# Performance work log

Hardware: AMD Instinct MI355X
Metric: run time of the kernel (lower is better)

Reference implementation:

```python
import jax, jax.numpy as jnp
import numpy as np

D_MODEL = 1024
N_HEADS = 16
D_K = D_MODEL // N_HEADS
B, S = 4, 2048


def _xavier(key, out_dim, in_dim):
    limit = float(np.sqrt(6.0 / (in_dim + out_dim)))
    return jax.random.uniform(key, (out_dim, in_dim), jnp.float32, -limit, limit)


def setup_inputs() -> dict:
    key = jax.random.key(0)
    ks = jax.random.split(key, 7)
    return {
        "query": jax.random.normal(ks[0], (B, S, D_MODEL), jnp.float32),
        "key": jax.random.normal(ks[1], (B, S, D_MODEL), jnp.float32),
        "value": jax.random.normal(ks[2], (B, S, D_MODEL), jnp.float32),
        "W_q": _xavier(ks[3], D_MODEL, D_MODEL), "b_q": jnp.zeros((D_MODEL,), jnp.float32),
        "W_k": _xavier(ks[4], D_MODEL, D_MODEL), "b_k": jnp.zeros((D_MODEL,), jnp.float32),
        "W_v": _xavier(ks[5], D_MODEL, D_MODEL), "b_v": jnp.zeros((D_MODEL,), jnp.float32),
        "W_o": _xavier(ks[6], D_MODEL, D_MODEL), "b_o": jnp.zeros((D_MODEL,), jnp.float32),
    }


def reference(query, key, value, W_q, b_q, W_k, b_k, W_v, b_v, W_o, b_o):
    b, sq, _ = query.shape
    sk = key.shape[1]
    # Linear projections (torch Linear: x @ W.T + b), then split heads -> (b, h, s, d_k)
    Q = (query @ W_q.T + b_q).reshape(b, sq, N_HEADS, D_K).transpose(0, 2, 1, 3)
    K = (key @ W_k.T + b_k).reshape(b, sk, N_HEADS, D_K).transpose(0, 2, 1, 3)
    V = (value @ W_v.T + b_v).reshape(b, sk, N_HEADS, D_K).transpose(0, 2, 1, 3)
    # Naive full-score attention: (b, h, sq, sk) materialized, as in the original
    scores = jnp.einsum("bhqd,bhkd->bhqk", Q, K) / jnp.sqrt(jnp.float32(D_K))
    attn = jax.nn.softmax(scores, axis=-1)
    out = jnp.einsum("bhqk,bhkd->bhqd", attn, V)
    out = out.transpose(0, 2, 1, 3).reshape(b, sq, D_MODEL)
    return out @ W_o.T + b_o
```

## Files before the change

### kernel.cpp

```cpp
#include <hip/hip_runtime.h>
#include <hip/hip_bf16.h>
#include <cstdint>
#include <cstddef>

typedef unsigned short u16;
typedef unsigned int u32;
typedef __attribute__((ext_vector_type(8))) short bf16x8;
typedef __attribute__((ext_vector_type(4))) float f32x4;
typedef __attribute__((ext_vector_type(16))) float f32x16;
typedef __attribute__((ext_vector_type(4))) unsigned int u32x4;
typedef __attribute__((ext_vector_type(4))) unsigned short u16x4;

#define MFMA16(A,B,C) __builtin_amdgcn_mfma_f32_16x16x32_bf16(A,B,C,0,0,0)
#define MFMA32(A,B,C) __builtin_amdgcn_mfma_f32_32x32x16_bf16(A,B,C,0,0,0)

__device__ __forceinline__ u16 f2bf(float x) {
  __hip_bfloat16 h = __float2bfloat16(x);
  return __builtin_bit_cast(u16, h);
}

__device__ __forceinline__ float fast_exp2(float x) {
  float r;
  asm("v_exp_f32 %0, %1" : "=v"(r) : "v"(x));
  return r;
}

__device__ __forceinline__ void async_copy16(u16* lds, const u16* g) {
  __builtin_amdgcn_global_load_lds(
      (const __attribute__((address_space(1))) void*)g,
      (__attribute__((address_space(3))) void*)lds, 16, 0, 0);
}

__global__ void cvt4_kernel(const float* __restrict__ i0, const float* __restrict__ i1,
                            const float* __restrict__ i2, const float* __restrict__ i3,
                            u16* __restrict__ o0, u16* __restrict__ o1,
                            u16* __restrict__ o2, u16* __restrict__ o3, int n4) {
  const float* in; u16* out;
  switch (blockIdx.y) {
    case 0:  in = i0; out = o0; break;
    case 1:  in = i1; out = o1; break;
    case 2:  in = i2; out = o2; break;
    default: in = i3; out = o3; break;
  }
  int i = blockIdx.x * blockDim.x + threadIdx.x;
  int stride = gridDim.x * blockDim.x;
  for (; i < n4; i += stride) {
    float4 v = reinterpret_cast<const float4*>(in)[i];
    u16x4 o;
    o.x = f2bf(v.x); o.y = f2bf(v.y); o.z = f2bf(v.z); o.w = f2bf(v.w);
    reinterpret_cast<u16x4*>(out)[i] = o;
  }
}

template<bool BF16OUT>
__global__ __launch_bounds__(256, 2)
void gemm_nt_bias(const u16* __restrict__ A, const u16* __restrict__ W,
                  const float* __restrict__ bias, void* __restrict__ Cout,
                  int M, int N, int K, float scale) {
  __shared__ __attribute__((aligned(16))) u16 As[2][128*32];
  __shared__ __attribute__((aligned(16))) u16 Bs[2][128*32];
  const int t = threadIdx.x;
  const int lane = t & 63, wid = t >> 6;
  const int wr = wid >> 1, wc = wid & 1;
  const int g = lane >> 4, qc = lane & 15;
  const size_t m0 = (size_t)blockIdx.x * 128;
  const size_t n0 = (size_t)blockIdx.y * 128;
  f32x4 acc[4][4] = {};

#define GSTAGE(buf, k0_) do {                                         \
    _Pragma("unroll")                                                 \
    for (int c = 0; c < 2; ++c) {                                     \
      int s = c*256 + t;                                              \
      int row = s >> 2, ch = s & 3;                                   \
      int sch = ch ^ ((row >> 1) & 3);                                \
      async_copy16(&As[buf][s*8], &A[(m0 + row)*K + (k0_) + sch*8]);  \
    }                                                                 \
    _Pragma("unroll")                                                 \
    for (int c = 0; c < 2; ++c) {                                     \
      int s = c*256 + t;                                              \
      int row = s >> 2, ch = s & 3;                                   \
      int sch = ch ^ ((row >> 1) & 3);                                \
      async_copy16(&Bs[buf][s*8], &W[(n0 + row)*K + (k0_) + sch*8]);  \
    }                                                                 \
  } while (0)

  GSTAGE(0, 0);
  int cur = 0;
  for (int k0 = 0; k0 < K; k0 += 32) {
    __syncthreads();
    if (k0 + 32 < K) GSTAGE(cur ^ 1, k0 + 32);
    bf16x8 af[4], bfr[4];
    #pragma unroll
    for (int i = 0; i < 4; ++i) {
      int r = wr*64 + i*16 + qc;
      int ch = g ^ ((r >> 1) & 3);
      af[i] = *reinterpret_cast<const bf16x8*>(&As[cur][r*32 + ch*8]);
    }
    #pragma unroll
    for (int j = 0; j < 4; ++j) {
      int r = wc*64 + j*16 + qc;
      int ch = g ^ ((r >> 1) & 3);
      bfr[j] = *reinterpret_cast<const bf16x8*>(&Bs[cur][r*32 + ch*8]);
    }
    #pragma unroll
    for (int i = 0; i < 4; ++i)
      #pragma unroll
      for (int j = 0; j < 4; ++j)
        acc[i][j] = MFMA16(af[i], bfr[j], acc[i][j]);
    cur ^= 1;
  }
#undef GSTAGE

  #pragma unroll
  for (int j = 0; j < 4; ++j) {
    size_t col = n0 + wc*64 + j*16 + qc;
    float bv = bias[col];
    #pragma unroll
    for (int i = 0; i < 4; ++i) {
      #pragma unroll
      for (int r = 0; r < 4; ++r) {
        size_t row = m0 + wr*64 + i*16 + g*4 + r;
        float v = (acc[i][j][r] + bv) * scale;
        if (BF16OUT) ((u16*)Cout)[row*N + col] = f2bf(v);
        else         ((float*)Cout)[row*N + col] = v;
      }
    }
  }
}

__global__ __launch_bounds__(512, 4)
void flash_attn3(const u16* __restrict__ Qp, const u16* __restrict__ Kp,
                 const u16* __restrict__ Vp, u16* __restrict__ O) {
  __shared__ __attribute__((aligned(16))) u16 Ks[2][64*64];
  __shared__ __attribute__((aligned(16))) u16 Vt[3][64*64];
  const int t = threadIdx.x;
  const int w = t >> 6, lane = t & 63;
  const int l31 = lane & 31, hi = lane >> 5;
  const int bh = blockIdx.x;
  const size_t rowbase = (size_t)(bh >> 4) * 2048;
  const int hoff = (bh & 15) * 64;
  const int q0 = blockIdx.y * 256 + w * 32;
  const float THR = 11.5415603f;

  bf16x8 bq[4];
  {
    const u16* qp = &Qp[(rowbase + q0 + l31) * 1024 + hoff + hi * 8];
    #pragma unroll
    for (int dd = 0; dd < 4; ++dd) bq[dd] = *reinterpret_cast<const bf16x8*>(qp + dd*16);
  }

  f32x16 accO[2] = {};
  float m_run = 0.f, l_run = 0.f;
  u32 pwp[2][8];

  const int kvr_s = t >> 3, c_s = t & 7;
  const int sc_s = c_s ^ ((kvr_s >> 3) & 7);
  const int vd0_s = (t & 7) * 8;
  const int vcs = kvr_s >> 3;

  async_copy16(&Ks[0][t*8], &Kp[(rowbase + kvr_s)*1024 + hoff + sc_s*8]);
  bf16x8 vreg = *reinterpret_cast<const bf16x8*>(&Vp[(rowbase + kvr_s)*1024 + hoff + vd0_s]);

  int wi = 0, ri = 2;
  for (int kv = 0; kv < 32; ++kv) {
    const int kb = kv & 1;
    u16* vw = &Vt[0][0] + wi*4096;
    const u16* vrd = &Vt[0][0] + ri*4096;

    #pragma unroll
    for (int j = 0; j < 8; ++j) {
      int d = vd0_s + j;
      vw[d*64 + ((vcs ^ ((d>>3)&7))*8) + (kvr_s & 7)] = (u16)vreg[j];
    }
    __syncthreads();
    if (kv < 31) {
      const size_t nb = rowbase + (size_t)(kv+1)*64;
      async_copy16(&Ks[kb^1][t*8], &Kp[(nb + kvr_s)*1024 + hoff + sc_s*8]);
      vreg = *reinterpret_cast<const bf16x8*>(&Vp[(nb + kvr_s)*1024 + hoff + vd0_s]);
    }

    f32x16 sacc[2];
    {
      const float negm = -m_run;
      #pragma unroll
      for (int i = 0; i < 16; ++i) { sacc[0][i] = negm; sacc[1][i] = negm; }
    }
    #pragma unroll
    for (int n = 0; n < 2; ++n) {
      int kvr = n*32 + l31;
      int swz = (kvr >> 3) & 7;
      #pragma unroll
      for (int dd = 0; dd < 4; ++dd) {
        int ch = (2*dd + hi) ^ swz;
        bf16x8 ak = *reinterpret_cast<const bf16x8*>(&Ks[kb][kvr*64 + ch*8]);
        sacc[n] = MFMA32(ak, bq[dd], sacc[n]);
      }
    }

    if (kv > 0) {
      #pragma unroll
      for (int ks = 0; ks < 4; ++ks) {
        const int n = ks >> 1, kp = ks & 1;
        u32 wA0 = pwp[n][4*kp+0], wA1 = pwp[n][4*kp+1];
        u32 wB0 = pwp[n][4*kp+2], wB1 = pwp[n][4*kp+3];
        u32 s0 = hi ? wA0 : wB0, s1 = hi ? wA1 : wB1;
        u32 r0 = (u32)__shfl_xor((int)s0, 32);
        u32 r1 = (u32)__shfl_xor((int)s1, 32);
        u32 k0 = hi ? wB0 : wA0, k1 = hi ? wB1 : wA1;
        u32x4 fu;
        fu.x = hi ? r0 : k0; fu.y = hi ? r1 : k1;
        fu.z = hi ? k0 : r0; fu.w = hi ? k1 : r1;
        bf16x8 pa = __builtin_bit_cast(bf16x8, fu);
        #pragma unroll
        for (int dt = 0; dt < 2; ++dt) {
          int d = dt*32 + l31;
          int ch = (2*ks + hi) ^ ((d>>3)&7);
          bf16x8 bv = *reinterpret_cast<const bf16x8*>(&vrd[d*64 + ch*8]);
          accO[dt] = MFMA32(pa, bv, accO[dt]);
        }
      }
    }

    float a0 = fmaxf(fmaxf(sacc[0][0],sacc[0][1]),sacc[0][2]);
    float a1 = fmaxf(fmaxf(sacc[0][3],sacc[0][4]),sacc[0][5]);
    float a2 = fmaxf(fmaxf(sacc[0][6],sacc[0][7]),sacc[0][8]);
    float a3 = fmaxf(fmaxf(sacc[0][9],sacc[0][10]),sacc[0][11]);
    float a4 = fmaxf(fmaxf(sacc[0][12],sacc[0][13]),sacc[0][14]);
    float a5 = fmaxf(fmaxf(sacc[0][15],sacc[1][0]),sacc[1][1]);
    float a6 = fmaxf(fmaxf(sacc[1][2],sacc[1][3]),sacc[1][4]);
    float a7 = fmaxf(fmaxf(sacc[1][5],sacc[1][6]),sacc[1][7]);
    float a8 = fmaxf(fmaxf(sacc[1][8],sacc[1][9]),sacc[1][10]);
    float a9 = fmaxf(fmaxf(sacc[1][11],sacc[1][12]),sacc[1][13]);
    float aA = fmaxf(sacc[1][14],sacc[1][15]);
    float b0 = fmaxf(fmaxf(a0,a1),a2);
    float b1 = fmaxf(fmaxf(a3,a4),a5);
    float b2 = fmaxf(fmaxf(a6,a7),a8);
    float b3 = fmaxf(a9,aA);
    float mloc = fmaxf(fmaxf(b0,b1),fmaxf(b2,b3));
    float mx = fmaxf(mloc, __shfl_xor(mloc, 32));

    if (__any(mx > THR)) {
      float dm = fmaxf(mx, 0.f);
      float alpha = fast_exp2(-dm);
      m_run += dm;
      l_run *= alpha;
      #pragma unroll
      for (int n = 0; n < 2; ++n)
        #pragma unroll
        for (int r = 0; r < 16; ++r) sacc[n][r] -= dm;
      #pragma unroll
      for (int r = 0; r < 16; ++r) {
        int qrow = (r&3) + 8*(r>>2) + 4*hi;
        float ar = __shfl(alpha, qrow);
        accO[0][r] *= ar; accO[1][r] *= ar;
      }
    }

    #pragma unroll
    for (int n = 0; n < 2; ++n)
      #pragma unroll
      for (int r = 0; r < 16; ++r) sacc[n][r] = fast_exp2(sacc[n][r]);
    #pragma unroll
    for (int n = 0; n < 2; ++n)
      #pragma unroll
      for (int i = 0; i < 8; ++i)
        pwp[n][i] = (u32)f2bf(sacc[n][2*i]) | ((u32)f2bf(sacc[n][2*i+1]) << 16);
    float ts[16];
    #pragma unroll
    for (int i = 0; i < 16; ++i) ts[i] = sacc[0][i] + sacc[1][i];
    #pragma unroll
    for (int off = 8; off >= 1; off >>= 1)
      #pragma unroll
      for (int i = 0; i < off; ++i) ts[i] += ts[i + off];
    l_run += ts[0] + __shfl_xor(ts[0], 32);

    wi = (wi == 2) ? 0 : wi + 1;
    ri = (ri == 2) ? 0 : ri + 1;
  }

  {
    const u16* vrd = &Vt[0][0] + ri*4096;
    #pragma unroll
    for (int ks = 0; ks < 4; ++ks) {
      const int n = ks >> 1, kp = ks & 1;
      u32 wA0 = pwp[n][4*kp+0], wA1 = pwp[n][4*kp+1];
      u32 wB0 = pwp[n][4*kp+2], wB1 = pwp[n][4*kp+3];
      u32 s0 = hi ? wA0 : wB0, s1 = hi ? wA1 : wB1;
      u32 r0 = (u32)__shfl_xor((int)s0, 32);
      u32 r1 = (u32)__shfl_xor((int)s1, 32);
      u32 k0 = hi ? wB0 : wA0, k1 = hi ? wB1 : wA1;
      u32x4 fu;
      fu.x = hi ? r0 : k0; fu.y = hi ? r1 : k1;
      fu.z = hi ? k0 : r0; fu.w = hi ? k1 : r1;
      bf16x8 pa = __builtin_bit_cast(bf16x8, fu);
      #pragma unroll
      for (int dt = 0; dt < 2; ++dt) {
        int d = dt*32 + l31;
        int ch = (2*ks + hi) ^ ((d>>3)&7);
        bf16x8 bv = *reinterpret_cast<const bf16x8*>(&vrd[d*64 + ch*8]);
        accO[dt] = MFMA32(pa, bv, accO[dt]);
      }
    }
  }

  float linv = 1.0f / l_run;
  #pragma unroll
  for (int r = 0; r < 16; ++r) {
    int qrow = (r&3) + 8*(r>>2) + 4*hi;
    float lv = __shfl(linv, qrow);
    size_t orow = rowbase + q0 + qrow;
    O[orow*1024 + hoff + l31]      = f2bf(accO[0][r] * lv);
    O[orow*1024 + hoff + 32 + l31] = f2bf(accO[1][r] * lv);
  }
}

extern "C" void kernel_launch(void* const* d_in, const int* in_sizes, int n_in,
                              void* d_out, int out_size, void* d_ws, size_t ws_size,
                              hipStream_t stream) {
  (void)in_sizes; (void)n_in; (void)out_size; (void)ws_size;
  const float* query = (const float*)d_in[0];
  const float* key   = (const float*)d_in[1];
  const float* value = (const float*)d_in[2];
  const float* W_q   = (const float*)d_in[3];
  const float* b_q   = (const float*)d_in[4];
  const float* W_k   = (const float*)d_in[5];
  const float* b_k   = (const float*)d_in[6];
  const float* W_v   = (const float*)d_in[7];
  const float* b_v   = (const float*)d_in[8];
  const float* W_o   = (const float*)d_in[9];
  const float* b_o   = (const float*)d_in[10];

  const size_t sz_t = (size_t)8192 * 1024;
  const size_t sz_w = (size_t)1024 * 1024;
  u16* ws = (u16*)d_ws;
  u16* xq = ws;
  u16* xk = ws + 1*sz_t;
  u16* xv = ws + 2*sz_t;
  u16* Qp = ws + 3*sz_t;
  u16* Kp = ws + 4*sz_t;
  u16* Vp = ws + 5*sz_t;
  u16* wq = ws + 6*sz_t;
  u16* wk = wq + sz_w;
  u16* wv = wq + 2*sz_w;
  u16* wo = wq + 3*sz_w;

  const float SCL = 0.125f * 1.44269504089f;

  cvt4_kernel<<<dim3(512, 4), 256, 0, stream>>>(W_q, W_k, W_v, W_o,
                                                wq, wk, wv, wo, (int)(sz_w/4));
  cvt4_kernel<<<dim3(2048, 3), 256, 0, stream>>>(query, key, value, value,
                                                 xq, xk, xv, xv, (int)(sz_t/4));

  dim3 gg(8192/128, 1024/128);
  gemm_nt_bias<true><<<gg, 256, 0, stream>>>(xq, wq, b_q, Qp, 8192, 1024, 1024, SCL);
  gemm_nt_bias<true><<<gg, 256, 0, stream>>>(xk, wk, b_k, Kp, 8192, 1024, 1024, 1.0f);
  gemm_nt_bias<true><<<gg, 256, 0, stream>>>(xv, wv, b_v, Vp, 8192, 1024, 1024, 1.0f);

  flash_attn3<<<dim3(64, 8), 512, 0, stream>>>(Qp, Kp, Vp, xq);

  gemm_nt_bias<false><<<gg, 256, 0, stream>>>(xq, wo, b_o, d_out, 8192, 1024, 1024, 1.0f);
}
```

Before: 244.5 us.

## Merge QKV projections into one launch and use 8-wave GEMM blocks

The three Q/K/V projection GEMMs become a single launch that picks its operands from blockIdx.z, giving one 1536-block grid in place of three 512-block grids. The GEMM body now uses 512 threads (8 waves), each computing a 64x32 sub-tile instead of 64x64, and each thread issues one async copy per operand per stage. This is meant to cut launch and tail overhead and raise the number of waves available to hide latency. In exchange, each block loads more LDS fragments per MFMA and has more waves contending at every barrier.

```diff
diff --git a/kernel.cpp b/kernel.cpp
--- a/kernel.cpp
+++ b/kernel.cpp
@@ -53,35 +53,25 @@
 }
 
 template<bool BF16OUT>
-__global__ __launch_bounds__(256, 2)
-void gemm_nt_bias(const u16* __restrict__ A, const u16* __restrict__ W,
-                  const float* __restrict__ bias, void* __restrict__ Cout,
-                  int M, int N, int K, float scale) {
+__device__ __forceinline__ void gemm_body(const u16* __restrict__ A, const u16* __restrict__ W,
+                                          const float* __restrict__ bias, void* __restrict__ Cout,
+                                          int N, int K, float scale) {
   __shared__ __attribute__((aligned(16))) u16 As[2][128*32];
   __shared__ __attribute__((aligned(16))) u16 Bs[2][128*32];
   const int t = threadIdx.x;
   const int lane = t & 63, wid = t >> 6;
-  const int wr = wid >> 1, wc = wid & 1;
+  const int wr = wid >> 2, wc = wid & 3;
   const int g = lane >> 4, qc = lane & 15;
   const size_t m0 = (size_t)blockIdx.x * 128;
   const size_t n0 = (size_t)blockIdx.y * 128;
-  f32x4 acc[4][4] = {};
-
-#define GSTAGE(buf, k0_) do {                                         \
-    _Pragma("unroll")                                                 \
-    for (int c = 0; c < 2; ++c) {                                     \
-      int s = c*256 + t;                                              \
-      int row = s >> 2, ch = s & 3;                                   \
-      int sch = ch ^ ((row >> 1) & 3);                                \
-      async_copy16(&As[buf][s*8], &A[(m0 + row)*K + (k0_) + sch*8]);  \
-    }                                                                 \
-    _Pragma("unroll")                                                 \
-    for (int c = 0; c < 2; ++c) {                                     \
-      int s = c*256 + t;                                              \
-      int row = s >> 2, ch = s & 3;                                   \
-      int sch = ch ^ ((row >> 1) & 3);                                \
-      async_copy16(&Bs[buf][s*8], &W[(n0 + row)*K + (k0_) + sch*8]);  \
-    }                                                                 \
+  f32x4 acc[4][2] = {};
+
+  const int srow = t >> 2;
+  const int ssch = (t & 3) ^ ((srow >> 1) & 3);
+
+#define GSTAGE(buf, k0_) do {                                            \
+    async_copy16(&As[buf][t*8], &A[(m0 + srow)*K + (k0_) + ssch*8]);     \
+    async_copy16(&Bs[buf][t*8], &W[(n0 + srow)*K + (k0_) + ssch*8]);     \
   } while (0)
 
   GSTAGE(0, 0);
@@ -89,7 +79,7 @@
   for (int k0 = 0; k0 < K; k0 += 32) {
     __syncthreads();
     if (k0 + 32 < K) GSTAGE(cur ^ 1, k0 + 32);
-    bf16x8 af[4], bfr[4];
+    bf16x8 af[4], bfr[2];
     #pragma unroll
     for (int i = 0; i < 4; ++i) {
       int r = wr*64 + i*16 + qc;
@@ -97,23 +87,23 @@
       af[i] = *reinterpret_cast<const bf16x8*>(&As[cur][r*32 + ch*8]);
     }
     #pragma unroll
-    for (int j = 0; j < 4; ++j) {
-      int r = wc*64 + j*16 + qc;
+    for (int j = 0; j < 2; ++j) {
+      int r = wc*32 + j*16 + qc;
       int ch = g ^ ((r >> 1) & 3);
       bfr[j] = *reinterpret_cast<const bf16x8*>(&Bs[cur][r*32 + ch*8]);
     }
     #pragma unroll
     for (int i = 0; i < 4; ++i)
       #pragma unroll
-      for (int j = 0; j < 4; ++j)
+      for (int j = 0; j < 2; ++j)
         acc[i][j] = MFMA16(af[i], bfr[j], acc[i][j]);
     cur ^= 1;
   }
 #undef GSTAGE
 
   #pragma unroll
-  for (int j = 0; j < 4; ++j) {
-    size_t col = n0 + wc*64 + j*16 + qc;
+  for (int j = 0; j < 2; ++j) {
+    size_t col = n0 + wc*32 + j*16 + qc;
     float bv = bias[col];
     #pragma unroll
     for (int i = 0; i < 4; ++i) {
@@ -126,6 +116,28 @@
       }
     }
   }
+}
+
+__global__ __launch_bounds__(512, 2)
+void gemm_qkv(const u16* __restrict__ xq, const u16* __restrict__ xk,
+              const u16* __restrict__ xv, const u16* __restrict__ wq,
+              const u16* __restrict__ wk, const u16* __restrict__ wv,
+              const float* __restrict__ b_q, const float* __restrict__ b_k,
+              const float* __restrict__ b_v, u16* __restrict__ Qp,
+              u16* __restrict__ Kp, u16* __restrict__ Vp, float scaleQ) {
+  const u16* A; const u16* W; const float* bias; u16* C; float scale;
+  switch (blockIdx.z) {
+    case 0:  A = xq; W = wq; bias = b_q; C = Qp; scale = scaleQ; break;
+    case 1:  A = xk; W = wk; bias = b_k; C = Kp; scale = 1.0f;   break;
+    default: A = xv; W = wv; bias = b_v; C = Vp; scale = 1.0f;   break;
+  }
+  gemm_body<true>(A, W, bias, C, 1024, 1024, scale);
+}
+
+__global__ __launch_bounds__(512, 2)
+void gemm_out(const u16* __restrict__ A, const u16* __restrict__ W,
+              const float* __restrict__ bias, float* __restrict__ C) {
+  gemm_body<false>(A, W, bias, C, 1024, 1024, 1.0f);
 }
 
 __global__ __launch_bounds__(512, 4)
@@ -351,12 +363,10 @@
   cvt4_kernel<<<dim3(2048, 3), 256, 0, stream>>>(query, key, value, value,
                                                  xq, xk, xv, xv, (int)(sz_t/4));
 
-  dim3 gg(8192/128, 1024/128);
-  gemm_nt_bias<true><<<gg, 256, 0, stream>>>(xq, wq, b_q, Qp, 8192, 1024, 1024, SCL);
-  gemm_nt_bias<true><<<gg, 256, 0, stream>>>(xk, wk, b_k, Kp, 8192, 1024, 1024, 1.0f);
-  gemm_nt_bias<true><<<gg, 256, 0, stream>>>(xv, wv, b_v, Vp, 8192, 1024, 1024, 1.0f);
+  gemm_qkv<<<dim3(8192/128, 1024/128, 3), 512, 0, stream>>>(
+      xq, xk, xv, wq, wk, wv, b_q, b_k, b_v, Qp, Kp, Vp, SCL);
 
   flash_attn3<<<dim3(64, 8), 512, 0, stream>>>(Qp, Kp, Vp, xq);
 
-  gemm_nt_bias<false><<<gg, 256, 0, stream>>>(xq, wo, b_o, d_out, 8192, 1024, 1024, 1.0f);
-}
+  gemm_out<<<dim3(8192/128, 1024/128), 512, 0, stream>>>(xq, wo, b_o, (float*)d_out);
+}
```

Measured after the change: 229.2 us. -6.2%, faster.
